# Kernel optimization log

Measured on AMD Instinct MI355X. Metric: run time of the kernel, lower is better.

The kernel has to match this reference:

```python
import jax, jax.numpy as jnp
import numpy as np

H, D_MODEL, D_K, D_V = 16, 1024, 64, 64
B, L = 4, 2048

def _linear_params(key, in_dim, out_dim):
    kw, kb = jax.random.split(key)
    bound = 1.0 / np.sqrt(in_dim)
    W = jax.random.uniform(kw, (out_dim, in_dim), jnp.float32, -bound, bound)
    b = jax.random.uniform(kb, (out_dim,), jnp.float32, -bound, bound)
    return W, b

def setup_inputs() -> dict:
    key = jax.random.key(0)
    ks = jax.random.split(key, 7)
    V = jax.random.normal(ks[0], (B, L, D_MODEL), jnp.float32)
    K = jax.random.normal(ks[1], (B, L, D_MODEL), jnp.float32)
    Q = jax.random.normal(ks[2], (B, L, D_MODEL), jnp.float32)
    Wv, bv = _linear_params(ks[3], D_MODEL, H * D_V)
    Wk, bk = _linear_params(ks[4], D_MODEL, H * D_K)
    Wq, bq = _linear_params(ks[5], D_MODEL, H * D_K)
    Wo, bo = _linear_params(ks[6], H * D_V, D_MODEL)
    return {"V": V, "K": K, "Q": Q, "Wv": Wv, "bv": bv, "Wk": Wk, "bk": bk,
            "Wq": Wq, "bq": bq, "Wo": Wo, "bo": bo}

def reference(V, K, Q, Wv, bv, Wk, bk, Wq, bq, Wo, bo):
    batch, len1, _ = V.shape
    len2 = Q.shape[1]
    # project and split heads: (b, l, h, d)
    v = (V @ Wv.T + bv).reshape(batch, len1, H, D_V)
    k = (K @ Wk.T + bk).reshape(batch, len1, H, D_K)
    q = (Q @ Wq.T + bq).reshape(batch, len2, H, D_K)
    scale = 1.0 / jnp.sqrt(jnp.asarray(D_K, q.dtype))
    # scores: (b, h, len2, len1)
    scores = jnp.einsum('bqhd,bkhd->bhqk', q, k) * scale
    attn = jax.nn.softmax(scores, axis=-1)
    out = jnp.einsum('bhqk,bkhd->bqhd', attn, v).reshape(batch, len2, H * D_V)
    return out @ Wo.T + bo
```

## Files before the change

### kernel.cpp

```cpp
#include <hip/hip_runtime.h>


typedef __bf16 bf16;
typedef __attribute__((ext_vector_type(8))) __bf16 bf16x8;
typedef __attribute__((ext_vector_type(4))) __bf16 bf16x4;
typedef __attribute__((ext_vector_type(4))) float f32x4;
typedef __attribute__((ext_vector_type(16))) float f32x16;

__global__ __launch_bounds__(256) void cvt_all(
    const float* __restrict__ Q, const float* __restrict__ K, const float* __restrict__ V,
    const float* __restrict__ Wq, const float* __restrict__ Wk,
    const float* __restrict__ Wv, const float* __restrict__ Wo,
    bf16* __restrict__ ws)
{
    int bid = blockIdx.x;
    const float* src;
    bf16* dst;
    int lb;
    if (bid < 4096)       { src = Q;  dst = ws;             lb = bid; }
    else if (bid < 8192)  { src = K;  dst = ws + 8388608;   lb = bid - 4096; }
    else if (bid < 12288) { src = V;  dst = ws + 16777216;  lb = bid - 8192; }
    else if (bid < 12800) { src = Wq; dst = ws + 25165824;  lb = bid - 12288; }
    else if (bid < 13312) { src = Wk; dst = ws + 26214400;  lb = bid - 12800; }
    else if (bid < 13824) { src = Wv; dst = ws + 27262976;  lb = bid - 13312; }
    else                  { src = Wo; dst = ws + 28311552;  lb = bid - 13824; }
    size_t i = ((size_t)lb * 256 + threadIdx.x) * 8;
    f32x4 a = *(const f32x4*)(src + i);
    f32x4 b = *(const f32x4*)(src + i + 4);
    bf16x8 o;
    o[0] = (bf16)a[0]; o[1] = (bf16)a[1]; o[2] = (bf16)a[2]; o[3] = (bf16)a[3];
    o[4] = (bf16)b[0]; o[5] = (bf16)b[1]; o[6] = (bf16)b[2]; o[7] = (bf16)b[3];
    *(bf16x8*)(dst + i) = o;
}

__device__ inline void gld_lds16(const void* g, void* l) {
    __builtin_amdgcn_global_load_lds((const __attribute__((address_space(1))) void*)g,
                                     (__attribute__((address_space(3))) void*)l, 16, 0, 0);
}

__global__ __launch_bounds__(256) void proj_fused(
    const bf16* __restrict__ Xq, const bf16* __restrict__ Xk, const bf16* __restrict__ Xv,
    const bf16* __restrict__ Wqb, const bf16* __restrict__ Wkb, const bf16* __restrict__ Wvb,
    const float* __restrict__ bq, const float* __restrict__ bk, const float* __restrict__ bv,
    bf16* __restrict__ qw, bf16* __restrict__ kw, bf16* __restrict__ vtw)
{
    __shared__ bf16 lA[2][4096];
    __shared__ bf16 lB[2][4096];
    const int z = blockIdx.z;
    const bf16*  A    = z == 0 ? Xq  : (z == 1 ? Xk  : Xv);
    const bf16*  W    = z == 0 ? Wqb : (z == 1 ? Wkb : Wvb);
    const float* bias = z == 0 ? bq  : (z == 1 ? bk  : bv);
    bf16*        out  = z == 0 ? qw  : (z == 1 ? kw  : vtw);
    const float scale = z == 0 ? 0.18033688011112042f : 1.0f;

    const int tid  = threadIdx.x;
    const int wave = tid >> 6, lane = tid & 63;
    const int c = lane & 15, g = lane >> 4;
    const int m0 = blockIdx.y * 128, n0 = blockIdx.x * 128;
    const int wr = wave >> 1, wc = wave & 1;
    const int srow = lane >> 2;
    const int scol = (lane & 3) * 8;

    f32x4 acc[4][4] = {};

#define PSTAGE(kt_, bb)                                                         \
    {                                                                           \
        _Pragma("unroll")                                                       \
        for (int h = 0; h < 2; ++h) {                                           \
            int ca = wave + h * 4;                                              \
            int arow = ca * 16 + srow;                                          \
            gld_lds16(A + (size_t)(m0 + arow) * 1024 + (kt_) * 32 + scol,       \
                      &lA[bb][ca * 512]);                                       \
            gld_lds16(W + (size_t)(n0 + arow) * 1024 + (kt_) * 32 + scol,       \
                      &lB[bb][ca * 512]);                                       \
        }                                                                       \
    }

    PSTAGE(0, 0);
    asm volatile("s_waitcnt vmcnt(0)" ::: "memory");
    __syncthreads();

    int buf = 0;
    for (int kt = 0; kt < 32; ++kt) {
        if (kt + 1 < 32) PSTAGE(kt + 1, buf ^ 1);

        bf16x8 af[4], bfr[4];
#pragma unroll
        for (int m = 0; m < 4; ++m)
            af[m] = *(const bf16x8*)&lA[buf][(wr * 64 + m * 16 + c) * 32 + g * 8];
#pragma unroll
        for (int n = 0; n < 4; ++n)
            bfr[n] = *(const bf16x8*)&lB[buf][(wc * 64 + n * 16 + c) * 32 + g * 8];
#pragma unroll
        for (int m = 0; m < 4; ++m)
#pragma unroll
            for (int n = 0; n < 4; ++n)
                acc[m][n] = __builtin_amdgcn_mfma_f32_16x16x32_bf16(af[m], bfr[n], acc[m][n], 0, 0, 0);

        asm volatile("s_waitcnt vmcnt(0)" ::: "memory");
        __syncthreads();
        buf ^= 1;
    }
#undef PSTAGE

#pragma unroll
    for (int m = 0; m < 4; ++m) {
#pragma unroll
        for (int n = 0; n < 4; ++n) {
            int col  = n0 + wc * 64 + n * 16 + c;
            float bb = bias[col];
#pragma unroll
            for (int r = 0; r < 4; ++r) {
                int row = m0 + wr * 64 + m * 16 + 4 * g + r;
                float v = (acc[m][n][r] + bb) * scale;
                int b = row >> 11, l = row & 2047, hh = col >> 6, d = col & 63;
                size_t base = (size_t)(b * 16 + hh) * 131072;
                if (z < 2) {
                    out[base + (l >> 5) * 2048 + (d >> 4) * 512 +
                        ((d >> 3) & 1) * 256 + (l & 31) * 8 + (d & 7)] = (bf16)v;
                } else {
                    out[base + (l >> 5) * 2048 + (d >> 5) * 1024 +
                        ((l >> 4) & 1) * 512 + ((l >> 3) & 1) * 256 +
                        (d & 31) * 8 + (l & 7)] = (bf16)v;
                }
            }
        }
    }
}

__global__ __launch_bounds__(256) void gemm_out(
    const bf16* __restrict__ A, const bf16* __restrict__ W,
    const float* __restrict__ bias, float* __restrict__ out)
{
    __shared__ bf16 lA[2][4096];
    __shared__ bf16 lB[2][4096];
    const int tid  = threadIdx.x;
    const int wave = tid >> 6, lane = tid & 63;
    const int c = lane & 15, g = lane >> 4;
    const int m0 = blockIdx.y * 128, n0 = blockIdx.x * 128;
    const int wr = wave >> 1, wc = wave & 1;
    const int srow = lane >> 2;
    const int scol = (lane & 3) * 8;

    f32x4 acc[4][4] = {};

#define OSTAGE(kt_, bb)                                                         \
    {                                                                           \
        _Pragma("unroll")                                                       \
        for (int h = 0; h < 2; ++h) {                                           \
            int ca = wave + h * 4;                                              \
            int arow = ca * 16 + srow;                                          \
            gld_lds16(A + (size_t)(m0 + arow) * 1024 + (kt_) * 32 + scol,       \
                      &lA[bb][ca * 512]);                                       \
            gld_lds16(W + (size_t)(n0 + arow) * 1024 + (kt_) * 32 + scol,       \
                      &lB[bb][ca * 512]);                                       \
        }                                                                       \
    }

    OSTAGE(0, 0);
    asm volatile("s_waitcnt vmcnt(0)" ::: "memory");
    __syncthreads();

    int buf = 0;
    for (int kt = 0; kt < 32; ++kt) {
        if (kt + 1 < 32) OSTAGE(kt + 1, buf ^ 1);

        bf16x8 af[4], bfr[4];
#pragma unroll
        for (int m = 0; m < 4; ++m)
            af[m] = *(const bf16x8*)&lA[buf][(wr * 64 + m * 16 + c) * 32 + g * 8];
#pragma unroll
        for (int n = 0; n < 4; ++n)
            bfr[n] = *(const bf16x8*)&lB[buf][(wc * 64 + n * 16 + c) * 32 + g * 8];
#pragma unroll
        for (int m = 0; m < 4; ++m)
#pragma unroll
            for (int n = 0; n < 4; ++n)
                acc[m][n] = __builtin_amdgcn_mfma_f32_16x16x32_bf16(af[m], bfr[n], acc[m][n], 0, 0, 0);

        asm volatile("s_waitcnt vmcnt(0)" ::: "memory");
        __syncthreads();
        buf ^= 1;
    }
#undef OSTAGE

#pragma unroll
    for (int m = 0; m < 4; ++m) {
#pragma unroll
        for (int n = 0; n < 4; ++n) {
            int col  = n0 + wc * 64 + n * 16 + c;
            float bb = bias[col];
#pragma unroll
            for (int r = 0; r < 4; ++r) {
                int row = m0 + wr * 64 + m * 16 + 4 * g + r;
                out[(size_t)row * 1024 + col] = acc[m][n][r] + bb;
            }
        }
    }
}

__device__ inline unsigned cvtpk(float lo, float hi) {
    unsigned r;
    asm("v_cvt_pk_bf16_f32 %0, %1, %2" : "=v"(r) : "v"(lo), "v"(hi));
    return r;
}
__device__ inline void pswap(unsigned &a, unsigned &b) {
    asm("v_permlane32_swap_b32 %0, %1" : "+v"(a), "+v"(b));
}

__global__ __launch_bounds__(512) void attn_kernel(
    const bf16* __restrict__ q, const bf16* __restrict__ k,
    const bf16* __restrict__ vt, bf16* __restrict__ O)
{
    __shared__ bf16 lkv[3][4096];
    const int tid  = threadIdx.x;
    const int wave = tid >> 6, lane = tid & 63;
    const int l31 = lane & 31, hi = lane >> 5;
    const int orig = blockIdx.x;
    const int swz  = (orig & 7) * 64 + (orig >> 3);
    const int bh = swz >> 3;
    const int q0 = (swz & 7) * 256 + wave * 32;
    const int laneoff = hi * 256 + l31 * 8;

    const bf16* qb = q  + (size_t)bh * 131072 + (q0 >> 5) * 2048 + laneoff;
    const bf16* kb = k  + (size_t)bh * 131072;
    const bf16* vb = vt + (size_t)bh * 131072;

    bf16x8 qf0 = *(const bf16x8*)(qb);
    bf16x8 qf1 = *(const bf16x8*)(qb + 512);
    bf16x8 qf2 = *(const bf16x8*)(qb + 1024);
    bf16x8 qf3 = *(const bf16x8*)(qb + 1536);

    const bf16* sg = (wave < 4) ? (kb + wave * 512 + lane * 8)
                                : (vb + (wave - 4) * 512 + lane * 8);
    const int   sl = (wave < 4) ? wave * 512 : 2048 + (wave - 4) * 512;

    bf16x8 ones;
#pragma unroll
    for (int i = 0; i < 8; ++i) ones[i] = (bf16)1.0f;

    f32x16 acc0 = {}, acc1 = {}, accS = {};

    gld_lds16(sg,        &lkv[0][sl]);
    gld_lds16(sg + 2048, &lkv[1][sl]);

    int cur = 0;
    for (int t = 0; t < 64; ++t) {
        if (t < 62) {
            int nb = cur + 2; if (nb >= 3) nb -= 3;
            gld_lds16(sg + (size_t)(t + 2) * 2048, &lkv[nb][sl]);
            asm volatile("s_waitcnt vmcnt(2)" ::: "memory");
        } else if (t == 62) {
            asm volatile("s_waitcnt vmcnt(1)" ::: "memory");
        } else {
            asm volatile("s_waitcnt vmcnt(0)" ::: "memory");
        }
        __syncthreads();

        const bf16* kl = &lkv[cur][laneoff];
        const bf16* vl = &lkv[cur][2048 + laneoff];
        bf16x8 kf0  = *(const bf16x8*)(kl);
        bf16x8 kf1  = *(const bf16x8*)(kl + 512);
        bf16x8 kf2  = *(const bf16x8*)(kl + 1024);
        bf16x8 kf3  = *(const bf16x8*)(kl + 1536);
        bf16x8 vf00 = *(const bf16x8*)(vl);
        bf16x8 vf01 = *(const bf16x8*)(vl + 512);
        bf16x8 vf10 = *(const bf16x8*)(vl + 1024);
        bf16x8 vf11 = *(const bf16x8*)(vl + 1536);

        f32x16 st = {};
        __builtin_amdgcn_s_setprio(1);
        st = __builtin_amdgcn_mfma_f32_32x32x16_bf16(kf0, qf0, st, 0, 0, 0);
        st = __builtin_amdgcn_mfma_f32_32x32x16_bf16(kf1, qf1, st, 0, 0, 0);
        st = __builtin_amdgcn_mfma_f32_32x32x16_bf16(kf2, qf2, st, 0, 0, 0);
        st = __builtin_amdgcn_mfma_f32_32x32x16_bf16(kf3, qf3, st, 0, 0, 0);
        __builtin_amdgcn_s_setprio(0);

#pragma unroll
        for (int r = 0; r < 16; ++r) st[r] = __builtin_amdgcn_exp2f(st[r]);

        unsigned u01 = cvtpk(st[0],  st[1]),  u23 = cvtpk(st[2],  st[3]);
        unsigned u45 = cvtpk(st[4],  st[5]),  u67 = cvtpk(st[6],  st[7]);
        unsigned u89 = cvtpk(st[8],  st[9]),  uAB = cvtpk(st[10], st[11]);
        unsigned uCD = cvtpk(st[12], st[13]), uEF = cvtpk(st[14], st[15]);
        pswap(u01, u45); pswap(u23, u67);
        pswap(u89, uCD); pswap(uAB, uEF);
        union { unsigned u[4]; bf16x8 v; } pf0, pf1;
        pf0.u[0] = u01; pf0.u[1] = u23; pf0.u[2] = u45; pf0.u[3] = u67;
        pf1.u[0] = u89; pf1.u[1] = uAB; pf1.u[2] = uCD; pf1.u[3] = uEF;

        __builtin_amdgcn_s_setprio(1);
        acc0 = __builtin_amdgcn_mfma_f32_32x32x16_bf16(vf00, pf0.v, acc0, 0, 0, 0);
        acc1 = __builtin_amdgcn_mfma_f32_32x32x16_bf16(vf10, pf0.v, acc1, 0, 0, 0);
        accS = __builtin_amdgcn_mfma_f32_32x32x16_bf16(ones, pf0.v, accS, 0, 0, 0);
        acc0 = __builtin_amdgcn_mfma_f32_32x32x16_bf16(vf01, pf1.v, acc0, 0, 0, 0);
        acc1 = __builtin_amdgcn_mfma_f32_32x32x16_bf16(vf11, pf1.v, acc1, 0, 0, 0);
        accS = __builtin_amdgcn_mfma_f32_32x32x16_bf16(ones, pf1.v, accS, 0, 0, 0);
        __builtin_amdgcn_s_setprio(0);

        __syncthreads();
        cur = (cur == 2) ? 0 : cur + 1;
    }

    float inv = 1.0f / accS[0];
    int qg = q0 + l31;
    bf16* ob = O + ((size_t)(bh >> 4) * 2048 + qg) * 1024 + (size_t)(bh & 15) * 64;
#pragma unroll
    for (int rg = 0; rg < 4; ++rg) {
        bf16x4 w0, w1;
#pragma unroll
        for (int i = 0; i < 4; ++i) {
            w0[i] = (bf16)(acc0[rg * 4 + i] * inv);
            w1[i] = (bf16)(acc1[rg * 4 + i] * inv);
        }
        *(bf16x4*)(ob + 8 * rg + 4 * hi)      = w0;
        *(bf16x4*)(ob + 32 + 8 * rg + 4 * hi) = w1;
    }
}

extern "C" void kernel_launch(void* const* d_in, const int* in_sizes, int n_in,
                              void* d_out, int out_size, void* d_ws, size_t ws_size,
                              hipStream_t stream) {
    (void)in_sizes; (void)n_in; (void)out_size; (void)ws_size;
    const float* V  = (const float*)d_in[0];
    const float* K  = (const float*)d_in[1];
    const float* Q  = (const float*)d_in[2];
    const float* Wv = (const float*)d_in[3];
    const float* bv = (const float*)d_in[4];
    const float* Wk = (const float*)d_in[5];
    const float* bk = (const float*)d_in[6];
    const float* Wq = (const float*)d_in[7];
    const float* bq = (const float*)d_in[8];
    const float* Wo = (const float*)d_in[9];
    const float* bo = (const float*)d_in[10];

    char* ws = (char*)d_ws;
    const size_t MB = 1ull << 20;
    bf16* Xq  = (bf16*)(ws + 0);
    bf16* Xk  = (bf16*)(ws + 16 * MB);
    bf16* Xv  = (bf16*)(ws + 32 * MB);
    bf16* Wqb = (bf16*)(ws + 48 * MB);
    bf16* Wkb = (bf16*)(ws + 50 * MB);
    bf16* Wvb = (bf16*)(ws + 52 * MB);
    bf16* Wob = (bf16*)(ws + 54 * MB);
    bf16* qw  = (bf16*)(ws + 56 * MB);
    bf16* kw  = (bf16*)(ws + 72 * MB);
    bf16* vtw = (bf16*)(ws + 88 * MB);
    bf16* Ow  = (bf16*)(ws + 0);

    cvt_all<<<14336, 256, 0, stream>>>(Q, K, V, Wq, Wk, Wv, Wo, (bf16*)ws);

    proj_fused<<<dim3(8, 64, 3), 256, 0, stream>>>(
        Xq, Xk, Xv, Wqb, Wkb, Wvb, bq, bk, bv, qw, kw, vtw);

    attn_kernel<<<512, 512, 0, stream>>>(qw, kw, vtw, Ow);

    gemm_out<<<dim3(8, 64), 256, 0, stream>>>(Ow, Wob, bo, (float*)d_out);
}
```

Baseline: 221.6 us.

## Triple-buffer GEMM LDS staging with partial waits, XOR swizzle, and tile remap

In both projection and output GEMMs, LDS staging goes from double to triple buffering with two tiles in flight, using partial vmcnt waits instead of draining all loads each iteration. The global-to-LDS column offsets and the fragment reads use an XOR swizzle to cut LDS bank conflicts. Block indices are remapped so consecutive blocks share A/W tiles in cache. The cost is more LDS per block (48KB), which may lower occupancy, and correctness depends on the hand-tuned vmcnt counts.

After: 200.3 us. 1.11x faster.

```diff
diff --git a/kernel.cpp b/kernel.cpp
--- a/kernel.cpp
+++ b/kernel.cpp
@@ -38,14 +38,16 @@
                                      (__attribute__((address_space(3))) void*)l, 16, 0, 0);
 }
 
+__device__ inline int swz4(int r) { return (r & 3) ^ ((r >> 2) & 3); }
+
 __global__ __launch_bounds__(256) void proj_fused(
     const bf16* __restrict__ Xq, const bf16* __restrict__ Xk, const bf16* __restrict__ Xv,
     const bf16* __restrict__ Wqb, const bf16* __restrict__ Wkb, const bf16* __restrict__ Wvb,
     const float* __restrict__ bq, const float* __restrict__ bk, const float* __restrict__ bv,
     bf16* __restrict__ qw, bf16* __restrict__ kw, bf16* __restrict__ vtw)
 {
-    __shared__ bf16 lA[2][4096];
-    __shared__ bf16 lB[2][4096];
+    __shared__ bf16 lA[3][4096];
+    __shared__ bf16 lB[3][4096];
     const int z = blockIdx.z;
     const bf16*  A    = z == 0 ? Xq  : (z == 1 ? Xk  : Xv);
     const bf16*  W    = z == 0 ? Wqb : (z == 1 ? Wkb : Wvb);
@@ -56,10 +58,15 @@
     const int tid  = threadIdx.x;
     const int wave = tid >> 6, lane = tid & 63;
     const int c = lane & 15, g = lane >> 4;
-    const int m0 = blockIdx.y * 128, n0 = blockIdx.x * 128;
+
+    const int oid = blockIdx.y * 8 + blockIdx.x;
+    const int nid = (oid & 7) * 64 + (oid >> 3);
+    const int m0 = (nid >> 3) * 128, n0 = (nid & 7) * 128;
+
     const int wr = wave >> 1, wc = wave & 1;
-    const int srow = lane >> 2;
-    const int scol = (lane & 3) * 8;
+    const int srow  = lane >> 2;
+    const int sscol = (((lane & 3) ^ swz4(srow)) * 8);
+    const int rdsw  = (g ^ swz4(c)) * 8;
 
     f32x4 acc[4][4] = {};
 
@@ -69,37 +76,45 @@
         for (int h = 0; h < 2; ++h) {                                           \
             int ca = wave + h * 4;                                              \
             int arow = ca * 16 + srow;                                          \
-            gld_lds16(A + (size_t)(m0 + arow) * 1024 + (kt_) * 32 + scol,       \
+            gld_lds16(A + (size_t)(m0 + arow) * 1024 + (kt_) * 32 + sscol,      \
                       &lA[bb][ca * 512]);                                       \
-            gld_lds16(W + (size_t)(n0 + arow) * 1024 + (kt_) * 32 + scol,       \
+            gld_lds16(W + (size_t)(n0 + arow) * 1024 + (kt_) * 32 + sscol,      \
                       &lB[bb][ca * 512]);                                       \
         }                                                                       \
     }
 
     PSTAGE(0, 0);
-    asm volatile("s_waitcnt vmcnt(0)" ::: "memory");
-    __syncthreads();
-
-    int buf = 0;
+    PSTAGE(1, 1);
+
     for (int kt = 0; kt < 32; ++kt) {
-        if (kt + 1 < 32) PSTAGE(kt + 1, buf ^ 1);
+        const int buf = kt % 3;
+        if (kt + 2 < 32) {
+            PSTAGE(kt + 2, (kt + 2) % 3);
+            asm volatile("s_waitcnt vmcnt(8)" ::: "memory");
+        } else if (kt + 2 == 32) {
+            asm volatile("s_waitcnt vmcnt(4)" ::: "memory");
+        } else {
+            asm volatile("s_waitcnt vmcnt(0)" ::: "memory");
+        }
+        __builtin_amdgcn_s_barrier();
+        asm volatile("" ::: "memory");
 
         bf16x8 af[4], bfr[4];
 #pragma unroll
         for (int m = 0; m < 4; ++m)
-            af[m] = *(const bf16x8*)&lA[buf][(wr * 64 + m * 16 + c) * 32 + g * 8];
+            af[m] = *(const bf16x8*)&lA[buf][(wr * 4 + m) * 512 + c * 32 + rdsw];
 #pragma unroll
         for (int n = 0; n < 4; ++n)
-            bfr[n] = *(const bf16x8*)&lB[buf][(wc * 64 + n * 16 + c) * 32 + g * 8];
+            bfr[n] = *(const bf16x8*)&lB[buf][(wc * 4 + n) * 512 + c * 32 + rdsw];
 #pragma unroll
         for (int m = 0; m < 4; ++m)
 #pragma unroll
             for (int n = 0; n < 4; ++n)
                 acc[m][n] = __builtin_amdgcn_mfma_f32_16x16x32_bf16(af[m], bfr[n], acc[m][n], 0, 0, 0);
 
-        asm volatile("s_waitcnt vmcnt(0)" ::: "memory");
-        __syncthreads();
-        buf ^= 1;
+        asm volatile("" ::: "memory");
+        __builtin_amdgcn_s_barrier();
+        asm volatile("" ::: "memory");
     }
 #undef PSTAGE
 
@@ -132,15 +147,20 @@
     const bf16* __restrict__ A, const bf16* __restrict__ W,
     const float* __restrict__ bias, float* __restrict__ out)
 {
-    __shared__ bf16 lA[2][4096];
-    __shared__ bf16 lB[2][4096];
+    __shared__ bf16 lA[3][4096];
+    __shared__ bf16 lB[3][4096];
     const int tid  = threadIdx.x;
     const int wave = tid >> 6, lane = tid & 63;
     const int c = lane & 15, g = lane >> 4;
-    const int m0 = blockIdx.y * 128, n0 = blockIdx.x * 128;
+
+    const int oid = blockIdx.y * 8 + blockIdx.x;
+    const int nid = (oid & 7) * 64 + (oid >> 3);
+    const int m0 = (nid >> 3) * 128, n0 = (nid & 7) * 128;
+
     const int wr = wave >> 1, wc = wave & 1;
-    const int srow = lane >> 2;
-    const int scol = (lane & 3) * 8;
+    const int srow  = lane >> 2;
+    const int sscol = (((lane & 3) ^ swz4(srow)) * 8);
+    const int rdsw  = (g ^ swz4(c)) * 8;
 
     f32x4 acc[4][4] = {};
 
@@ -150,37 +170,45 @@
         for (int h = 0; h < 2; ++h) {                                           \
             int ca = wave + h * 4;                                              \
             int arow = ca * 16 + srow;                                          \
-            gld_lds16(A + (size_t)(m0 + arow) * 1024 + (kt_) * 32 + scol,       \
+            gld_lds16(A + (size_t)(m0 + arow) * 1024 + (kt_) * 32 + sscol,      \
                       &lA[bb][ca * 512]);                                       \
-            gld_lds16(W + (size_t)(n0 + arow) * 1024 + (kt_) * 32 + scol,       \
+            gld_lds16(W + (size_t)(n0 + arow) * 1024 + (kt_) * 32 + sscol,      \
                       &lB[bb][ca * 512]);                                       \
         }                                                                       \
     }
 
     OSTAGE(0, 0);
-    asm volatile("s_waitcnt vmcnt(0)" ::: "memory");
-    __syncthreads();
-
-    int buf = 0;
+    OSTAGE(1, 1);
+
     for (int kt = 0; kt < 32; ++kt) {
-        if (kt + 1 < 32) OSTAGE(kt + 1, buf ^ 1);
+        const int buf = kt % 3;
+        if (kt + 2 < 32) {
+            OSTAGE(kt + 2, (kt + 2) % 3);
+            asm volatile("s_waitcnt vmcnt(8)" ::: "memory");
+        } else if (kt + 2 == 32) {
+            asm volatile("s_waitcnt vmcnt(4)" ::: "memory");
+        } else {
+            asm volatile("s_waitcnt vmcnt(0)" ::: "memory");
+        }
+        __builtin_amdgcn_s_barrier();
+        asm volatile("" ::: "memory");
 
         bf16x8 af[4], bfr[4];
 #pragma unroll
         for (int m = 0; m < 4; ++m)
-            af[m] = *(const bf16x8*)&lA[buf][(wr * 64 + m * 16 + c) * 32 + g * 8];
+            af[m] = *(const bf16x8*)&lA[buf][(wr * 4 + m) * 512 + c * 32 + rdsw];
 #pragma unroll
         for (int n = 0; n < 4; ++n)
-            bfr[n] = *(const bf16x8*)&lB[buf][(wc * 64 + n * 16 + c) * 32 + g * 8];
+            bfr[n] = *(const bf16x8*)&lB[buf][(wc * 4 + n) * 512 + c * 32 + rdsw];
 #pragma unroll
         for (int m = 0; m < 4; ++m)
 #pragma unroll
             for (int n = 0; n < 4; ++n)
                 acc[m][n] = __builtin_amdgcn_mfma_f32_16x16x32_bf16(af[m], bfr[n], acc[m][n], 0, 0, 0);
 
-        asm volatile("s_waitcnt vmcnt(0)" ::: "memory");
-        __syncthreads();
-        buf ^= 1;
+        asm volatile("" ::: "memory");
+        __builtin_amdgcn_s_barrier();
+        asm volatile("" ::: "memory");
     }
 #undef OSTAGE
 
```

## Enlarge GEMM tiles to 256x256 with swizzled LDS and XCD-aware block mapping

Applied to the files above, without the earlier changes.

Both projection and output GEMMs move from 128x128 tiles with 4 waves to 256x256 tiles with 8 waves. Each wave now computes a 128x64 sub-tile, which raises MFMA work per LDS fragment load. The change also XOR-swizzles the LDS layout to cut bank conflicts, remaps block IDs so neighbouring tiles land on the same XCD, and uses a single barrier per k-step with setprio around the MFMAs. The cost is fewer blocks (384 and 128, against 256 CUs) and higher register and LDS use, so the output GEMM may underfill the GPU.

New measurement: 249.5 us. 12.6% more time.

```diff
diff --git a/kernel.cpp b/kernel.cpp
--- a/kernel.cpp
+++ b/kernel.cpp
@@ -38,15 +38,21 @@
                                      (__attribute__((address_space(3))) void*)l, 16, 0, 0);
 }
 
-__global__ __launch_bounds__(256) void proj_fused(
+__global__ __launch_bounds__(512, 2) void proj_fused(
     const bf16* __restrict__ Xq, const bf16* __restrict__ Xk, const bf16* __restrict__ Xv,
     const bf16* __restrict__ Wqb, const bf16* __restrict__ Wkb, const bf16* __restrict__ Wvb,
     const float* __restrict__ bq, const float* __restrict__ bk, const float* __restrict__ bv,
     bf16* __restrict__ qw, bf16* __restrict__ kw, bf16* __restrict__ vtw)
 {
-    __shared__ bf16 lA[2][4096];
-    __shared__ bf16 lB[2][4096];
-    const int z = blockIdx.z;
+    __shared__ bf16 lA[2][8192];
+    __shared__ bf16 lB[2][8192];
+
+    const int bid = blockIdx.x;
+    const int swz = (bid & 7) * 48 + (bid >> 3);
+    const int z   = swz >> 7;
+    const int rem = swz & 127;
+    const int m0 = (rem >> 2) * 256, n0 = (rem & 3) * 256;
+
     const bf16*  A    = z == 0 ? Xq  : (z == 1 ? Xk  : Xv);
     const bf16*  W    = z == 0 ? Wqb : (z == 1 ? Wkb : Wvb);
     const float* bias = z == 0 ? bq  : (z == 1 ? bk  : bv);
@@ -56,62 +62,63 @@
     const int tid  = threadIdx.x;
     const int wave = tid >> 6, lane = tid & 63;
     const int c = lane & 15, g = lane >> 4;
-    const int m0 = blockIdx.y * 128, n0 = blockIdx.x * 128;
-    const int wr = wave >> 1, wc = wave & 1;
+    const int wr = wave >> 2, wc = wave & 3;
+
     const int srow = lane >> 2;
-    const int scol = (lane & 3) * 8;
-
-    f32x4 acc[4][4] = {};
+    const int scol = ((lane & 3) ^ (lane >> 4)) * 8;
+    const int rsw  = (g ^ ((c >> 2) & 3)) * 8;
+
+    f32x4 acc[8][4] = {};
 
 #define PSTAGE(kt_, bb)                                                         \
     {                                                                           \
         _Pragma("unroll")                                                       \
         for (int h = 0; h < 2; ++h) {                                           \
-            int ca = wave + h * 4;                                              \
-            int arow = ca * 16 + srow;                                          \
-            gld_lds16(A + (size_t)(m0 + arow) * 1024 + (kt_) * 32 + scol,       \
-                      &lA[bb][ca * 512]);                                       \
-            gld_lds16(W + (size_t)(n0 + arow) * 1024 + (kt_) * 32 + scol,       \
-                      &lB[bb][ca * 512]);                                       \
+            int rbase = h * 128 + wave * 16;                                    \
+            gld_lds16(A + (size_t)(m0 + rbase + srow) * 1024 + (kt_) * 32 + scol, \
+                      &lA[bb][rbase * 32]);                                     \
+            gld_lds16(W + (size_t)(n0 + rbase + srow) * 1024 + (kt_) * 32 + scol, \
+                      &lB[bb][rbase * 32]);                                     \
         }                                                                       \
     }
 
     PSTAGE(0, 0);
-    asm volatile("s_waitcnt vmcnt(0)" ::: "memory");
-    __syncthreads();
-
-    int buf = 0;
+
     for (int kt = 0; kt < 32; ++kt) {
+        const int buf = kt & 1;
+        asm volatile("s_waitcnt vmcnt(0)" ::: "memory");
+        __builtin_amdgcn_sched_barrier(0);
+        __builtin_amdgcn_s_barrier();
+        __builtin_amdgcn_sched_barrier(0);
         if (kt + 1 < 32) PSTAGE(kt + 1, buf ^ 1);
 
-        bf16x8 af[4], bfr[4];
-#pragma unroll
-        for (int m = 0; m < 4; ++m)
-            af[m] = *(const bf16x8*)&lA[buf][(wr * 64 + m * 16 + c) * 32 + g * 8];
+        bf16x8 af[8], bfr[4];
+#pragma unroll
+        for (int m = 0; m < 8; ++m)
+            af[m] = *(const bf16x8*)&lA[buf][(wr * 128 + m * 16 + c) * 32 + rsw];
 #pragma unroll
         for (int n = 0; n < 4; ++n)
-            bfr[n] = *(const bf16x8*)&lB[buf][(wc * 64 + n * 16 + c) * 32 + g * 8];
-#pragma unroll
-        for (int m = 0; m < 4; ++m)
+            bfr[n] = *(const bf16x8*)&lB[buf][(wc * 64 + n * 16 + c) * 32 + rsw];
+
+        __builtin_amdgcn_s_setprio(1);
+#pragma unroll
+        for (int m = 0; m < 8; ++m)
 #pragma unroll
             for (int n = 0; n < 4; ++n)
                 acc[m][n] = __builtin_amdgcn_mfma_f32_16x16x32_bf16(af[m], bfr[n], acc[m][n], 0, 0, 0);
-
-        asm volatile("s_waitcnt vmcnt(0)" ::: "memory");
-        __syncthreads();
-        buf ^= 1;
+        __builtin_amdgcn_s_setprio(0);
     }
 #undef PSTAGE
 
 #pragma unroll
-    for (int m = 0; m < 4; ++m) {
+    for (int m = 0; m < 8; ++m) {
 #pragma unroll
         for (int n = 0; n < 4; ++n) {
             int col  = n0 + wc * 64 + n * 16 + c;
             float bb = bias[col];
 #pragma unroll
             for (int r = 0; r < 4; ++r) {
-                int row = m0 + wr * 64 + m * 16 + 4 * g + r;
+                int row = m0 + wr * 128 + m * 16 + 4 * g + r;
                 float v = (acc[m][n][r] + bb) * scale;
                 int b = row >> 11, l = row & 2047, hh = col >> 6, d = col & 63;
                 size_t base = (size_t)(b * 16 + hh) * 131072;
@@ -128,71 +135,77 @@
     }
 }
 
-__global__ __launch_bounds__(256) void gemm_out(
+__global__ __launch_bounds__(512, 2) void gemm_out(
     const bf16* __restrict__ A, const bf16* __restrict__ W,
     const float* __restrict__ bias, float* __restrict__ out)
 {
-    __shared__ bf16 lA[2][4096];
-    __shared__ bf16 lB[2][4096];
+    __shared__ bf16 lA[2][8192];
+    __shared__ bf16 lB[2][8192];
+
+    const int bid = blockIdx.x;
+    const int swz = (bid & 7) * 16 + (bid >> 3);
+    const int m0 = (swz >> 2) * 256, n0 = (swz & 3) * 256;
+
     const int tid  = threadIdx.x;
     const int wave = tid >> 6, lane = tid & 63;
     const int c = lane & 15, g = lane >> 4;
-    const int m0 = blockIdx.y * 128, n0 = blockIdx.x * 128;
-    const int wr = wave >> 1, wc = wave & 1;
+    const int wr = wave >> 2, wc = wave & 3;
+
     const int srow = lane >> 2;
-    const int scol = (lane & 3) * 8;
-
-    f32x4 acc[4][4] = {};
+    const int scol = ((lane & 3) ^ (lane >> 4)) * 8;
+    const int rsw  = (g ^ ((c >> 2) & 3)) * 8;
+
+    f32x4 acc[8][4] = {};
 
 #define OSTAGE(kt_, bb)                                                         \
     {                                                                           \
         _Pragma("unroll")                                                       \
         for (int h = 0; h < 2; ++h) {                                           \
-            int ca = wave + h * 4;                                              \
-            int arow = ca * 16 + srow;                                          \
-            gld_lds16(A + (size_t)(m0 + arow) * 1024 + (kt_) * 32 + scol,       \
-                      &lA[bb][ca * 512]);                                       \
-            gld_lds16(W + (size_t)(n0 + arow) * 1024 + (kt_) * 32 + scol,       \
-                      &lB[bb][ca * 512]);                                       \
+            int rbase = h * 128 + wave * 16;                                    \
+            gld_lds16(A + (size_t)(m0 + rbase + srow) * 1024 + (kt_) * 32 + scol, \
+                      &lA[bb][rbase * 32]);                                     \
+            gld_lds16(W + (size_t)(n0 + rbase + srow) * 1024 + (kt_) * 32 + scol, \
+                      &lB[bb][rbase * 32]);                                     \
         }                                                                       \
     }
 
     OSTAGE(0, 0);
-    asm volatile("s_waitcnt vmcnt(0)" ::: "memory");
-    __syncthreads();
-
-    int buf = 0;
+
     for (int kt = 0; kt < 32; ++kt) {
+        const int buf = kt & 1;
+        asm volatile("s_waitcnt vmcnt(0)" ::: "memory");
+        __builtin_amdgcn_sched_barrier(0);
+        __builtin_amdgcn_s_barrier();
+        __builtin_amdgcn_sched_barrier(0);
         if (kt + 1 < 32) OSTAGE(kt + 1, buf ^ 1);
 
-        bf16x8 af[4], bfr[4];
-#pragma unroll
-        for (int m = 0; m < 4; ++m)
-            af[m] = *(const bf16x8*)&lA[buf][(wr * 64 + m * 16 + c) * 32 + g * 8];
+        bf16x8 af[8], bfr[4];
+#pragma unroll
+        for (int m = 0; m < 8; ++m)
+            af[m] = *(const bf16x8*)&lA[buf][(wr * 128 + m * 16 + c) * 32 + rsw];
 #pragma unroll
         for (int n = 0; n < 4; ++n)
-            bfr[n] = *(const bf16x8*)&lB[buf][(wc * 64 + n * 16 + c) * 32 + g * 8];
-#pragma unroll
-        for (int m = 0; m < 4; ++m)
+            bfr[n] = *(const bf16x8*)&lB[buf][(wc * 64 + n * 16 + c) * 32 + rsw];
+
+        __builtin_amdgcn_s_setprio(1);
+#pragma unroll
+        for (int m = 0; m < 8; ++m)
 #pragma unroll
             for (int n = 0; n < 4; ++n)
                 acc[m][n] = __builtin_amdgcn_mfma_f32_16x16x32_bf16(af[m], bfr[n], acc[m][n], 0, 0, 0);
-
-        asm volatile("s_waitcnt vmcnt(0)" ::: "memory");
-        __syncthreads();
-        buf ^= 1;
+        __builtin_amdgcn_s_setprio(0);
     }
 #undef OSTAGE
 
 #pragma unroll
-    for (int m = 0; m < 4; ++m) {
+    for (int m = 0; m < 8; ++m) {
 #pragma unroll
         for (int n = 0; n < 4; ++n) {
             int col  = n0 + wc * 64 + n * 16 + c;
             float bb = bias[col];
 #pragma unroll
             for (int r = 0; r < 4; ++r) {
-                int row = m0 + wr * 64 + m * 16 + 4 * g + r;
+                int row = m0 + wr * 128 + m * 16 + 4 * g + r;
                 out[(size_t)row * 1024 + col] = acc[m][n][r] + bb;
             }
         }
@@ -350,10 +363,10 @@
 
     cvt_all<<<14336, 256, 0, stream>>>(Q, K, V, Wq, Wk, Wv, Wo, (bf16*)ws);
 
-    proj_fused<<<dim3(8, 64, 3), 256, 0, stream>>>(
+    proj_fused<<<384, 512, 0, stream>>>(
         Xq, Xk, Xv, Wqb, Wkb, Wvb, bq, bk, bv, qw, kw, vtw);
 
     attn_kernel<<<512, 512, 0, stream>>>(qw, kw, vtw, Ow);
 
-    gemm_out<<<dim3(8, 64), 256, 0, stream>>>(Ow, Wob, bo, (float*)d_out);
-}
+    gemm_out<<<128, 512, 0, stream>>>(Ow, Wob, bo, (float*)d_out);
+}
```
